# Optimization experiments

Measured on AMD Instinct MI355X. Metric: run time of the kernel, lower is better.

## Reference

```python
import jax, jax.numpy as jnp
import numpy as np


def setup_inputs() -> dict:
    key = jax.random.key(0)
    k1, k2 = jax.random.split(key)
    B, C, H, W = 8, 21, 512, 512
    inp = jax.random.normal(k1, (B, C, H, W), dtype=jnp.float32)
    target = jax.random.randint(k2, (B, H, W), 0, C, dtype=jnp.int64)
    return {"input": inp, "target": target}


def reference(input, target):
    # input: (B, C, H, W) logits; target: (B, H, W) int labels in [0, C)
    B, C, H, W = input.shape
    N = H * W
    logits = input.reshape(B, C, N)                      # (B, C, N)
    tgt = target.reshape(B, N)                           # (B, N)
    tgt_f = tgt.astype(logits.dtype)

    probs = jax.nn.softmax(logits, axis=1)               # (B, C, N)
    # foreground mask per class: (B, C, N)
    fg = (tgt[:, None, :] == jnp.arange(C)[None, :, None]).astype(logits.dtype)
    errors = jnp.abs(fg - probs)                         # (B, C, N)

    # descending sort along N, vectorized over all (B, C) rows
    perm = jnp.argsort(-errors, axis=2)                  # (B, C, N)
    errors_sorted = jnp.take_along_axis(errors, perm, axis=2)
    # faithful to kornia: gather the raw float labels (not the binary mask)
    tgt_bc = jnp.broadcast_to(tgt_f[:, None, :], (B, C, N))
    target_sorted = jnp.take_along_axis(tgt_bc, perm, axis=2)  # (B, C, N)

    tsum = jnp.sum(target_sorted, axis=2, keepdims=True)       # (B, C, 1)
    intersection = tsum - jnp.cumsum(target_sorted, axis=2)
    union = tsum + jnp.cumsum(1.0 - target_sorted, axis=2)
    gradient = 1.0 - intersection / union                      # (B, C, N)
    # in-place diff along last axis: g[..., 1:] -= g[..., :-1]
    gradient = jnp.concatenate(
        [gradient[..., :1], gradient[..., 1:] - gradient[..., :-1]], axis=-1
    )

    # per-class loss = mean over batch of sum over pixels; final = mean over classes
    loss_bc = jnp.sum(jax.nn.relu(errors_sorted) * gradient, axis=2)  # (B, C)
    return jnp.mean(loss_bc)
```

## Files before the change

kernel.cpp:

```cpp
#include <hip/hip_runtime.h>


#define NB    8
#define NC    21
#define NPIX  262144
#define NROWS (NB * NC)
#define NBINS 768
#define BPB   64
#define CHUNK (NPIX / BPB)

__global__ __launch_bounds__(512, 4) void k_fused(
    const float* __restrict__ x,
    const int* __restrict__ tgt,
    unsigned* __restrict__ partial) {
  __shared__ unsigned hist[NC * NBINS];
  int tid = threadIdx.x;
  for (int i = tid; i < NC * NBINS; i += 512) hist[i] = 0;
  __syncthreads();

  int b     = blockIdx.x >> 6;
  int chunk = blockIdx.x & 63;
  const float* xb = x + (size_t)b * NC * NPIX + (size_t)chunk * CHUNK;
  const int*   tb = tgt + (size_t)b * NPIX + (size_t)chunk * CHUNK;

  #pragma unroll
  for (int g = 0; g < 2; ++g) {
    int n4 = (g * 512 + tid) * 4;

    float v[NC][4];
    float m[4] = {-3.4e38f, -3.4e38f, -3.4e38f, -3.4e38f};
    #pragma unroll
    for (int c = 0; c < NC; ++c) {
      float4 t = *(const float4*)(xb + (size_t)c * NPIX + n4);
      v[c][0] = t.x; v[c][1] = t.y; v[c][2] = t.z; v[c][3] = t.w;
      m[0] = fmaxf(m[0], t.x); m[1] = fmaxf(m[1], t.y);
      m[2] = fmaxf(m[2], t.z); m[3] = fmaxf(m[3], t.w);
    }
    float Z[4] = {0.f, 0.f, 0.f, 0.f};
    #pragma unroll
    for (int c = 0; c < NC; ++c) {
      #pragma unroll
      for (int j = 0; j < 4; ++j) {
        v[c][j] = __expf(v[c][j] - m[j]);
        Z[j] += v[c][j];
      }
    }
    float iZ[4];
    #pragma unroll
    for (int j = 0; j < 4; ++j) iZ[j] = 1.0f / Z[j];

    int4 tv = *(const int4*)(tb + n4);
    int tl[4] = {tv.x, tv.y, tv.z, tv.w};

    #pragma unroll
    for (int c = 0; c < NC; ++c) {
      unsigned* hr = hist + c * NBINS;
      #pragma unroll
      for (int j = 0; j < 4; ++j) {
        float p = v[c][j] * iZ[j];
        float e = fabsf(((c == tl[j]) ? 1.0f : 0.0f) - p);
        unsigned fb   = __float_as_uint(e);
        int      fexp = (int)(fb >> 23) - 127;
        unsigned key;
        if (fexp < -12) key = 0u;
        else {
          key = (((unsigned)(fexp + 12)) << 6) | ((fb >> 17) & 63u);
          if (key > NBINS - 1) key = NBINS - 1;
        }
        atomicAdd(hr + key, (1u << 18) | (unsigned)tl[j]);
      }
    }
  }
  __syncthreads();

  unsigned* op = partial + (size_t)blockIdx.x * NC * NBINS;
  for (int i = tid; i < NC * NBINS; i += 512) op[i] = hist[i];
}

__device__ inline unsigned long long shfl_up_u64(unsigned long long v, int off) {
  unsigned lo = (unsigned)v, hi = (unsigned)(v >> 32);
  lo = (unsigned)__shfl_up((int)lo, off, 64);
  hi = (unsigned)__shfl_up((int)hi, off, 64);
  return ((unsigned long long)hi << 32) | lo;
}
__device__ inline unsigned long long shfl_down_u64(unsigned long long v, int off) {
  unsigned lo = (unsigned)v, hi = (unsigned)(v >> 32);
  lo = (unsigned)__shfl_down((int)lo, off, 64);
  hi = (unsigned)__shfl_down((int)hi, off, 64);
  return ((unsigned long long)hi << 32) | lo;
}

__global__ __launch_bounds__(768) void k_scan(
    const unsigned* __restrict__ partial,
    float* __restrict__ out) {
  int row  = blockIdx.x;
  int b    = row / NC;
  int c    = row - b * NC;
  int tid  = threadIdx.x;
  int lane = tid & 63;
  int wave = tid >> 6;

  __shared__ unsigned long long hist0[NBINS];
  __shared__ unsigned long long wtot[12];
  __shared__ double wred[12];
  __shared__ double sT;

  {
    const unsigned* pp = partial + ((size_t)(b * BPB) * NC + c) * NBINS + tid;
    unsigned long long cnt = 0, ls = 0;
    #pragma unroll 8
    for (int j = 0; j < BPB; ++j) {
      unsigned v = pp[(size_t)j * NC * NBINS];
      cnt += (v >> 18);
      ls  += (v & 0x3FFFFu);
    }
    hist0[tid] = (cnt << 32) | ls;
  }
  __syncthreads();

  unsigned long long tot = hist0[tid];
  #pragma unroll
  for (int off = 32; off > 0; off >>= 1) tot += shfl_down_u64(tot, off);
  if (lane == 0) wtot[wave] = tot;
  __syncthreads();
  if (tid == 0) {
    unsigned long long g = 0;
    #pragma unroll
    for (int w = 0; w < 12; ++w) g += wtot[w];
    sT = (double)(unsigned)(g & 0xffffffffULL);
  }
  __syncthreads();
  double T = sT;
  __syncthreads();

  int bin = (NBINS - 1) - tid;
  unsigned long long v = hist0[bin];

  unsigned long long s = v;
  #pragma unroll
  for (int off = 1; off < 64; off <<= 1) {
    unsigned long long u = shfl_up_u64(s, off);
    if (lane >= off) s += u;
  }
  if (lane == 63) wtot[wave] = s;
  __syncthreads();

  unsigned long long woff = 0;
  for (int w = 0; w < wave; ++w) woff += wtot[w];
  unsigned long long excl = s - v + woff;

  double acc = 0.0;
  unsigned n = (unsigned)(v >> 32);
  if (n) {
    unsigned sl = (unsigned)(v & 0xffffffffu);
    unsigned cb = (unsigned)(excl >> 32);
    unsigned sb = (unsigned)(excl & 0xffffffffu);
    double Sb = (double)sb + (double)sl;
    double gb = 1.0 - (T - Sb) / (T + (double)(cb + n) - Sb);
    double ga = (cb == 0) ? 0.0
                          : 1.0 - (T - (double)sb) / (T + (double)cb - (double)sb);
    unsigned key = (unsigned)bin;
    unsigned ex  = key >> 6, mant = key & 63u;
    float e = ldexpf(1.0f + ((float)mant + 0.5f) * 0.015625f, (int)ex - 12);
    acc = (double)e * (gb - ga);
  }

  #pragma unroll
  for (int off = 32; off > 0; off >>= 1) acc += __shfl_down(acc, off, 64);
  if (lane == 0) wred[wave] = acc;
  __syncthreads();
  if (tid == 0) {
    double ssum = 0.0;
    #pragma unroll
    for (int w = 0; w < 12; ++w) ssum += wred[w];
    atomicAdd(out, (float)(ssum * (1.0 / (double)NROWS)));
  }
}

extern "C" void kernel_launch(void* const* d_in, const int* in_sizes, int n_in,
                              void* d_out, int out_size, void* d_ws, size_t ws_size,
                              hipStream_t stream) {
  const float* x  = (const float*)d_in[0];
  const int* tgt  = (const int*)d_in[1];
  float* out      = (float*)d_out;
  unsigned* partial = (unsigned*)d_ws;

  hipMemsetAsync(d_out, 0, sizeof(float), stream);
  k_fused<<<NB * BPB, 512, 0, stream>>>(x, tgt, partial);
  k_scan<<<NROWS, NBINS, 0, stream>>>(partial, out);
}
```

Measured before the change: 271.2 us.

## Split softmax normalization from per-class histogram building to shrink LDS footprint

The single fused kernel is split in two. A new kernel computes a per-pixel log-sum-exp over the classes and writes it to workspace. The histogram kernel then assigns one class and one pixel chunk to each block, so it needs only a 768-bin LDS histogram instead of 21×768. This shrinks shared memory and register pressure, raising occupancy, and also halves the partial-histogram buffer the scan kernel reads. In exchange the logits are read from global memory twice and an extra per-pixel array is written and read back.

```diff
diff --git a/kernel.cpp b/kernel.cpp
--- a/kernel.cpp
+++ b/kernel.cpp
@@ -1,80 +1,81 @@
 #include <hip/hip_runtime.h>
 
 
-#define NB    8
-#define NC    21
-#define NPIX  262144
-#define NROWS (NB * NC)
-#define NBINS 768
-#define BPB   64
-#define CHUNK (NPIX / BPB)
+#define NB     8
+#define NC     21
+#define NPIX   262144
+#define NROWS  (NB * NC)
+#define NBINS  768
+#define CHUNKS 32
+#define HCHUNK (NPIX / CHUNKS)
 
-__global__ __launch_bounds__(512, 4) void k_fused(
+__global__ __launch_bounds__(256) void k_norm(
+    const float* __restrict__ x, float* __restrict__ L) {
+  int g = blockIdx.x * 256 + threadIdx.x;
+  int b = g >> 18;
+  const float* xp = x + (size_t)b * (NC - 1) * NPIX + g;
+  float v[NC];
+  float m = -3.4e38f;
+  #pragma unroll
+  for (int c = 0; c < NC; ++c) {
+    v[c] = xp[(size_t)c * NPIX];
+    m = fmaxf(m, v[c]);
+  }
+  float Z = 0.f;
+  #pragma unroll
+  for (int c = 0; c < NC; ++c) Z += __expf(v[c] - m);
+  L[g] = m + __logf(Z);
+}
+
+__global__ __launch_bounds__(256) void k_hist(
     const float* __restrict__ x,
     const int* __restrict__ tgt,
+    const float* __restrict__ L,
     unsigned* __restrict__ partial) {
-  __shared__ unsigned hist[NC * NBINS];
+  __shared__ unsigned hist[NBINS];
   int tid = threadIdx.x;
-  for (int i = tid; i < NC * NBINS; i += 512) hist[i] = 0;
+  int bid = blockIdx.x;
+  int c   = bid % NC;
+  int bc  = bid / NC;
+  int b   = bc / CHUNKS;
+  int ch  = bc - b * CHUNKS;
+
+  for (int i = tid; i < NBINS; i += 256) hist[i] = 0;
   __syncthreads();
 
-  int b     = blockIdx.x >> 6;
-  int chunk = blockIdx.x & 63;
-  const float* xb = x + (size_t)b * NC * NPIX + (size_t)chunk * CHUNK;
-  const int*   tb = tgt + (size_t)b * NPIX + (size_t)chunk * CHUNK;
+  int n0 = ch * HCHUNK;
+  const float* xb = x   + (size_t)(b * NC + c) * NPIX + n0;
+  const float* Lb = L   + (size_t)b * NPIX + n0;
+  const int*   tb = tgt + (size_t)b * NPIX + n0;
 
   #pragma unroll
-  for (int g = 0; g < 2; ++g) {
-    int n4 = (g * 512 + tid) * 4;
-
-    float v[NC][4];
-    float m[4] = {-3.4e38f, -3.4e38f, -3.4e38f, -3.4e38f};
+  for (int g = 0; g < 8; ++g) {
+    int n4 = (g * 256 + tid) * 4;
+    float4 xv = *(const float4*)(xb + n4);
+    float4 lv = *(const float4*)(Lb + n4);
+    int4   tv = *(const int4*)(tb + n4);
+    float xs[4] = {xv.x, xv.y, xv.z, xv.w};
+    float ls[4] = {lv.x, lv.y, lv.z, lv.w};
+    int   ts[4] = {tv.x, tv.y, tv.z, tv.w};
     #pragma unroll
-    for (int c = 0; c < NC; ++c) {
-      float4 t = *(const float4*)(xb + (size_t)c * NPIX + n4);
-      v[c][0] = t.x; v[c][1] = t.y; v[c][2] = t.z; v[c][3] = t.w;
-      m[0] = fmaxf(m[0], t.x); m[1] = fmaxf(m[1], t.y);
-      m[2] = fmaxf(m[2], t.z); m[3] = fmaxf(m[3], t.w);
-    }
-    float Z[4] = {0.f, 0.f, 0.f, 0.f};
-    #pragma unroll
-    for (int c = 0; c < NC; ++c) {
-      #pragma unroll
-      for (int j = 0; j < 4; ++j) {
-        v[c][j] = __expf(v[c][j] - m[j]);
-        Z[j] += v[c][j];
+    for (int j = 0; j < 4; ++j) {
+      float p = __expf(xs[j] - ls[j]);
+      float e = fabsf(((c == ts[j]) ? 1.0f : 0.0f) - p);
+      unsigned fb   = __float_as_uint(e);
+      int      fexp = (int)(fb >> 23) - 127;
+      unsigned key;
+      if (fexp < -12) key = 0u;
+      else {
+        key = (((unsigned)(fexp + 12)) << 6) | ((fb >> 17) & 63u);
+        if (key > NBINS - 1) key = NBINS - 1;
       }
-    }
-    float iZ[4];
-    #pragma unroll
-    for (int j = 0; j < 4; ++j) iZ[j] = 1.0f / Z[j];
-
-    int4 tv = *(const int4*)(tb + n4);
-    int tl[4] = {tv.x, tv.y, tv.z, tv.w};
-
-    #pragma unroll
-    for (int c = 0; c < NC; ++c) {
-      unsigned* hr = hist + c * NBINS;
-      #pragma unroll
-      for (int j = 0; j < 4; ++j) {
-        float p = v[c][j] * iZ[j];
-        float e = fabsf(((c == tl[j]) ? 1.0f : 0.0f) - p);
-        unsigned fb   = __float_as_uint(e);
-        int      fexp = (int)(fb >> 23) - 127;
-        unsigned key;
-        if (fexp < -12) key = 0u;
-        else {
-          key = (((unsigned)(fexp + 12)) << 6) | ((fb >> 17) & 63u);
-          if (key > NBINS - 1) key = NBINS - 1;
-        }
-        atomicAdd(hr + key, (1u << 18) | (unsigned)tl[j]);
-      }
+      atomicAdd(hist + key, (1u << 18) | (unsigned)ts[j]);
     }
   }
   __syncthreads();
 
-  unsigned* op = partial + (size_t)blockIdx.x * NC * NBINS;
-  for (int i = tid; i < NC * NBINS; i += 512) op[i] = hist[i];
+  unsigned* op = partial + (size_t)bid * NBINS;
+  for (int i = tid; i < NBINS; i += 256) op[i] = hist[i];
 }
 
 __device__ inline unsigned long long shfl_up_u64(unsigned long long v, int off) {
@@ -106,10 +107,10 @@
   __shared__ double sT;
 
   {
-    const unsigned* pp = partial + ((size_t)(b * BPB) * NC + c) * NBINS + tid;
+    const unsigned* pp = partial + ((size_t)(b * CHUNKS) * NC + c) * NBINS + tid;
     unsigned long long cnt = 0, ls = 0;
     #pragma unroll 8
-    for (int j = 0; j < BPB; ++j) {
+    for (int j = 0; j < CHUNKS; ++j) {
       unsigned v = pp[(size_t)j * NC * NBINS];
       cnt += (v >> 18);
       ls  += (v & 0x3FFFFu);
@@ -124,10 +125,10 @@
   if (lane == 0) wtot[wave] = tot;
   __syncthreads();
   if (tid == 0) {
-    unsigned long long g = 0;
+    unsigned long long gsum = 0;
     #pragma unroll
-    for (int w = 0; w < 12; ++w) g += wtot[w];
-    sT = (double)(unsigned)(g & 0xffffffffULL);
+    for (int w = 0; w < 12; ++w) gsum += wtot[w];
+    sT = (double)(unsigned)(gsum & 0xffffffffULL);
   }
   __syncthreads();
   double T = sT;
@@ -183,9 +184,11 @@
   const float* x  = (const float*)d_in[0];
   const int* tgt  = (const int*)d_in[1];
   float* out      = (float*)d_out;
-  unsigned* partial = (unsigned*)d_ws;
+  float* L        = (float*)d_ws;
+  unsigned* partial = (unsigned*)((char*)d_ws + (size_t)NB * NPIX * sizeof(float));
 
   hipMemsetAsync(d_out, 0, sizeof(float), stream);
-  k_fused<<<NB * BPB, 512, 0, stream>>>(x, tgt, partial);
+  k_norm<<<(NB * NPIX) / 256, 256, 0, stream>>>(x, L);
+  k_hist<<<NB * CHUNKS * NC, 256, 0, stream>>>(x, tgt, L, partial);
   k_scan<<<NROWS, NBINS, 0, stream>>>(partial, out);
 }
```

Result: slower. 298.1 us (+9.9%).
